# Optimization experiments

Hardware: AMD Instinct MI355X
Metric: run time of the kernel (lower is better)

Reference implementation:

```python
import jax, jax.numpy as jnp
import numpy as np

KS = 7
ITERS = 6
B, C, H, W = 2, 64, 256, 1216

_WM7 = [1,1,1,1,1,1,1,1,0,0,0,0,0,1,1,0,0,0,0,0,1,1,0,0,0,0,0,1,1,0,0,0,0,0,1,1,0,0,0,0,0,1,1,1,1,1,1,1,1]
_WM5 = [0,0,0,0,0,0,0,0,1,1,1,1,1,0,0,1,0,0,0,1,0,0,1,0,0,0,1,0,0,1,0,0,0,1,0,0,1,1,1,1,1,0,0,0,0,0,0,0,0]
_WM3 = [0,0,0,0,0,0,0,0,0,0,0,0,0,0,0,0,1,1,1,0,0,0,0,1,0,1,0,0,0,0,1,1,1,0,0,0,0,0,0,0,0,0,0,0,0,0,0,0,0]

# per 7x7 position t: which guide tensor (ring) and which channel within it
_SRC = []
_i7 = _i5 = _i3 = 0
for _t in range(KS * KS):
    if _WM7[_t]:
        _SRC.append(("7", _i7)); _i7 += 1
    elif _WM5[_t]:
        _SRC.append(("5", _i5)); _i5 += 1
    elif _WM3[_t]:
        _SRC.append(("3", _i3)); _i3 += 1
    else:
        _SRC.append(("1", 0))


def _convbn(x, w, s, b):
    # Conv2d(bias=False) + BatchNorm2d (inference) folded to per-channel scale/bias.
    y = jax.lax.conv_general_dilated(x, w, window_strides=(1, 1),
                                     padding=((1, 1), (1, 1)),
                                     dimension_numbers=("NCHW", "OIHW", "NCHW"))
    return y * s[None, :, None, None] + b[None, :, None, None]


def setup_inputs() -> dict:
    key = jax.random.key(0)
    ks = iter(jax.random.split(key, 64))
    def nrm(shape, scale=1.0):
        return jax.random.normal(next(ks), shape, jnp.float32) * scale
    def uni(shape):
        return jax.random.uniform(next(ks), shape, dtype=jnp.float32)
    inp = {
        "feature": nrm((B, C, H, W)),
        "d0": uni((B, 1, H, W)),
        "d00": nrm((B, 1, H, W)),  # ~half positive -> mixed valid_mask
    }
    layers = [("aff7", 24), ("aff5", 16), ("aff3", 8),
              ("att7", 6), ("att5", 6), ("att3", 6), ("att1", 6), ("mask", 6)]
    fan = 1.0 / np.sqrt(C * 9)
    for name, out in layers:
        inp["w_" + name] = nrm((out, C, 3, 3), fan)
        inp["s_" + name] = uni((out,))
        inp["b_" + name] = nrm((out,), 0.1)
    return inp


def reference(feature, d0, d00,
              w_aff7, s_aff7, b_aff7, w_aff5, s_aff5, b_aff5, w_aff3, s_aff3, b_aff3,
              w_att7, s_att7, b_att7, w_att5, s_att5, b_att5, w_att3, s_att3, b_att3,
              w_att1, s_att1, b_att1, w_mask, s_mask, b_mask):
    valid = (d00 > 0).astype(d00.dtype)
    mask_all = jax.nn.sigmoid(_convbn(feature, w_mask, s_mask, b_mask)) * valid
    aff7 = _convbn(feature, w_aff7, s_aff7, b_aff7)  # [B,24,H,W]
    aff5 = _convbn(feature, w_aff5, s_aff5, b_aff5)  # [B,16,H,W]
    aff3 = _convbn(feature, w_aff3, s_aff3, b_aff3)  # [B, 8,H,W]
    att7 = jax.nn.sigmoid(_convbn(feature, w_att7, s_att7, b_att7))
    att5 = jax.nn.sigmoid(_convbn(feature, w_att5, s_att5, b_att5))
    att3 = jax.nn.sigmoid(_convbn(feature, w_att3, s_att3, b_att3))
    att1 = jax.nn.sigmoid(_convbn(feature, w_att1, s_att1, b_att1))

    dt = d0
    for it in range(ITERS):
        mask = mask_all[:, it:it + 1]
        g7 = att7[:, it:it + 1] * aff7
        g5 = att5[:, it:it + 1] * aff5
        g3 = att3[:, it:it + 1] * aff3
        g1 = att1[:, it:it + 1]
        denom = (jnp.sum(jnp.abs(g7), 1, keepdims=True)
                 + jnp.sum(jnp.abs(g5), 1, keepdims=True)
                 + jnp.sum(jnp.abs(g3), 1, keepdims=True)
                 + jnp.abs(g1))
        g7, g5, g3, g1 = g7 / denom, g5 / denom, g3 / denom, g1 / denom
        g0 = 1.0 - (jnp.sum(g7, 1, keepdims=True) + jnp.sum(g5, 1, keepdims=True)
                    + jnp.sum(g3, 1, keepdims=True) + g1)
        guides = {"7": g7, "5": g5, "3": g3, "1": g1}
        # scatter ring guides into full 49-channel 7x7 layout
        G = jnp.concatenate([guides[k][:, i:i + 1] for k, i in _SRC], axis=1)  # [B,49,H,W]
        # weighted neighbor gather: out(p) = sum_t G_t(p+off_t) * dt(p+off_t)
        P = G * dt  # [B,49,H,W]
        Pp = jnp.pad(P, ((0, 0), (0, 0), (3, 3), (3, 3)))
        acc = jnp.zeros_like(dt)
        for t in range(KS * KS):
            i, j = t // KS, t % KS
            acc = acc + Pp[:, t:t + 1, 6 - i:6 - i + H, 6 - j:6 - j + W]
        dt = acc + g0 * d0
        dt = mask * d00 + (1.0 - mask) * dt
    return dt
```

## Files before the change

kernel.cpp:

```cpp
#include <hip/hip_runtime.h>
#include <hip/hip_fp16.h>
#include <stdint.h>

#define HH 256
#define WW 1216
#define BB 2
#define CC 64
#define IPIX (HH*WW)
#define NPIX (BB*IPIX)

typedef __attribute__((ext_vector_type(8))) __bf16 bf16x8;
typedef __attribute__((ext_vector_type(4))) __bf16 bf16x4;
typedef __attribute__((ext_vector_type(4))) float floatx4;
typedef __attribute__((ext_vector_type(4))) _Float16 half4;
typedef __attribute__((ext_vector_type(4))) uint32_t uint32x4;

__device__ __forceinline__ float sigm(float x) { return 1.f / (1.f + __expf(-x)); }

constexpr int LSTART_H[9] = {0,24,40,48,54,60,66,72,78};

constexpr int PLANE[49] = {
  0, 1, 2, 3, 4, 5, 6,
  7,24,25,26,27,28, 8,
  9,29,40,41,42,30,10,
 11,31,43,-1,44,32,12,
 13,33,45,46,47,34,14,
 15,35,36,37,38,39,16,
 17,18,19,20,21,22,23};
constexpr int KCLS[49] = {
 0,0,0,0,0,0,0,
 0,1,1,1,1,1,0,
 0,1,2,2,2,1,0,
 0,1,2,3,2,1,0,
 0,1,2,2,2,1,0,
 0,1,1,1,1,1,0,
 0,0,0,0,0,0,0};
constexpr int TAPNC[48] = {
  0,1,2,3,4,5,6,7,8,9,10,11,12,13,14,15,16,17,18,19,20,21,22,23,
  25,26,27,28,29,30,31,32,33,34,35,36,37,38,39,40,41,42,43,44,45,46,47,48};

struct WPtrs {
    const float* w[8];
    const float* s[8];
    const float* b[8];
};

__global__ void k_pack(WPtrs wp, __bf16* __restrict__ wpk,
                       float* __restrict__ s_all, float* __restrict__ b_all) {
    int idx = blockIdx.x * blockDim.x + threadIdx.x;
    if (idx < 18 * 5 * 64) {
        int kk = idx / (5 * 64);
        int r = idx - kk * 5 * 64;
        int t = r >> 6, lane = r & 63;
        int m = t * 16 + (lane & 15);
        int L = 0, o = 0;
        bool valid_m = (m < 78);
        if (valid_m) {
            for (int i = 0; i < 8; i++) if (m >= LSTART_H[i]) { L = i; o = m - LSTART_H[i]; }
        }
        __bf16 vals[8];
        for (int j = 0; j < 8; j++) {
            int k = kk * 32 + ((lane >> 4) * 8) + j;
            int tap = k >> 6, c = k & 63;
            float w = valid_m ? wp.w[L][(o * 64 + c) * 9 + tap] : 0.f;
            vals[j] = (__bf16)w;
        }
        for (int j = 0; j < 8; j++) wpk[(size_t)idx * 8 + j] = vals[j];
    }
    if (idx < 80) {
        int m = idx;
        float sv = 0.f, bv = 0.f;
        if (m < 78) {
            int L = 0, o = 0;
            for (int i = 0; i < 8; i++) if (m >= LSTART_H[i]) { L = i; o = m - LSTART_H[i]; }
            sv = wp.s[L][o]; bv = wp.b[L][o];
        }
        s_all[m] = sv; b_all[m] = bv;
    }
}

__global__ __launch_bounds__(256) void k_cvt(const float* __restrict__ feat,
                                             __bf16* __restrict__ fpk) {
    const int x = blockIdx.x * 64 + (threadIdx.x & 63);
    const int half = threadIdx.x >> 6;
    const int y = blockIdx.y, b = blockIdx.z;
    const float* fb = feat + (size_t)b * CC * IPIX + (size_t)y * WW + x;
    __bf16* op = fpk + ((size_t)(b * IPIX + y * WW + x) << 6);
#pragma unroll
    for (int h = 0; h < 2; h++) {
        const int cg = half + h * 4;
        bf16x8 pk;
#pragma unroll
        for (int j = 0; j < 8; j++) pk[j] = (__bf16)fb[(size_t)(cg * 8 + j) * IPIX];
        *(bf16x8*)(op + cg * 8) = pk;
    }
}

__global__ __launch_bounds__(256, 4) void k_conv(const __bf16* __restrict__ fpk,
        const float* __restrict__ d00, const __bf16* __restrict__ wpk,
        const float* __restrict__ s_all, const float* __restrict__ b_all,
        __bf16* __restrict__ afx, __bf16* __restrict__ attp, __bf16* __restrict__ maskp,
        float* __restrict__ stp) {
    __shared__ __bf16 sh[6 * 34 * 72];
    __shared__ __bf16 wlds[2 * 2560];
    const int tid = threadIdx.x;
    int flat = blockIdx.x + 38 * (blockIdx.y + 64 * blockIdx.z);
    int nf = (flat & 7) * 608 + (flat >> 3);
    int bx = nf % 38; int r2 = nf / 38;
    const int x0 = bx * 32, y0 = (r2 & 63) * 4, b = r2 >> 6;

    {
        bf16x8 w0 = *(const bf16x8*)(wpk + (size_t)tid * 8);
        *(bf16x8*)(wlds + tid * 8) = w0;
        if (tid < 64) {
            bf16x8 w1 = *(const bf16x8*)(wpk + 2048 + (size_t)tid * 8);
            *(bf16x8*)(wlds + 2048 + tid * 8) = w1;
        }
    }
    for (int idx = tid; idx < 204 * 8; idx += 256) {
        int cg = idx & 7, pos = idx >> 3;
        int row = pos / 34, x = pos - row * 34;
        int gy = y0 + row - 1, gx = x0 + x - 1;
        bf16x8 pk;
#pragma unroll
        for (int j = 0; j < 8; j++) pk[j] = (__bf16)0.f;
        if (gy >= 0 && gy < HH && gx >= 0 && gx < WW)
            pk = *(const bf16x8*)(fpk + ((size_t)(b * IPIX + gy * WW + gx) << 6) + cg * 8);
        *(bf16x8*)(sh + pos * 72 + cg * 8) = pk;
    }
    __syncthreads();

    const int wave = tid >> 6, lane = tid & 63;
    const int n = lane & 15, g = lane >> 4;

    floatx4 acc[5][2];
#pragma unroll
    for (int t = 0; t < 5; t++)
#pragma unroll
        for (int q = 0; q < 2; q++) acc[t][q] = (floatx4)(0.f);

#pragma unroll
    for (int kk = 0; kk < 18; kk++) {
        bf16x8 wt0, wt1;
        if (kk < 17) {
            wt0 = *(const bf16x8*)(wpk + (size_t)(kk + 1) * 2560 + tid * 8);
            if (tid < 64) wt1 = *(const bf16x8*)(wpk + (size_t)(kk + 1) * 2560 + 2048 + tid * 8);
        }
        const int tap = kk >> 1;
        const int dy = tap / 3 - 1, dx = tap % 3 - 1;
        const int c0 = (kk & 1) * 32 + g * 8;
        bf16x8 bfr[2];
        const int rowb = wave + 1 + dy;
        const int colb = 1 + dx + n;
#pragma unroll
        for (int q = 0; q < 2; q++)
            bfr[q] = *(const bf16x8*)(sh + ((rowb * 34) + colb + q * 16) * 72 + c0);
        bf16x8 afr[5];
        const __bf16* wb = wlds + (kk & 1) * 2560 + lane * 8;
#pragma unroll
        for (int t = 0; t < 5; t++) afr[t] = *(const bf16x8*)(wb + t * 512);
#pragma unroll
        for (int t = 0; t < 5; t++)
#pragma unroll
            for (int q = 0; q < 2; q++)
                acc[t][q] = __builtin_amdgcn_mfma_f32_16x16x32_bf16(afr[t], bfr[q], acc[t][q], 0, 0, 0);
        if (kk < 17) {
            *(bf16x8*)(wlds + ((kk + 1) & 1) * 2560 + tid * 8) = wt0;
            if (tid < 64) *(bf16x8*)(wlds + ((kk + 1) & 1) * 2560 + 2048 + tid * 8) = wt1;
        }
        __syncthreads();
    }

    const int pix_base = b * IPIX + (y0 + wave) * WW + x0 + n;
    float p7[2] = {0,0}, t7[2] = {0,0};
    float p5[2] = {0,0}, t5[2] = {0,0};
    float p3[2] = {0,0}, t3[2] = {0,0};

#pragma unroll
    for (int t = 0; t < 5; t++) {
        const floatx4 sv = *(const floatx4*)(s_all + t * 16 + 4 * g);
        const floatx4 bv = *(const floatx4*)(b_all + t * 16 + 4 * g);
#pragma unroll
        for (int q = 0; q < 2; q++) {
#pragma unroll
            for (int reg = 0; reg < 4; reg++) {
                const int m = t * 16 + 4 * g + reg;
                const float v = fmaf(acc[t][q][reg], sv[reg], bv[reg]);
                if (m < 24)                { p7[q] += fabsf(v); t7[q] += v; }
                else if (m < 40)           { p5[q] += fabsf(v); t5[q] += v; }
                else if (m < 48)           { p3[q] += fabsf(v); t3[q] += v; }
                const float outv = (m < 48) ? v : sigm(v);
                sh[m * 132 + wave * 32 + n + q * 16] = (__bf16)outv;
            }
        }
    }
#pragma unroll
    for (int q = 0; q < 2; q++) {
        p7[q] += __shfl_xor(p7[q], 16); p7[q] += __shfl_xor(p7[q], 32);
        t7[q] += __shfl_xor(t7[q], 16); t7[q] += __shfl_xor(t7[q], 32);
        p5[q] += __shfl_xor(p5[q], 16); p5[q] += __shfl_xor(p5[q], 32);
        t5[q] += __shfl_xor(t5[q], 16); t5[q] += __shfl_xor(t5[q], 32);
        p3[q] += __shfl_xor(p3[q], 16); p3[q] += __shfl_xor(p3[q], 32);
        t3[q] += __shfl_xor(t3[q], 16); t3[q] += __shfl_xor(t3[q], 32);
    }
    if (g == 0) {
#pragma unroll
        for (int q = 0; q < 2; q++) {
            const int pixq = pix_base + q * 16;
            floatx4 s0 = {p7[q], p5[q], p3[q], t7[q]};
            floatx4 s1 = {t5[q], t3[q], 0.f, 0.f};
            *(floatx4*)(stp + (size_t)pixq * 8)     = s0;
            *(floatx4*)(stp + (size_t)pixq * 8 + 4) = s1;
        }
    }
    __syncthreads();

    {
        const int pxi = tid >> 1;
        const int hf = tid & 1;
        const int prow2 = pxi >> 5, pcol2 = pxi & 31;
        const int pix2 = b * IPIX + (y0 + prow2) * WW + x0 + pcol2;
#pragma unroll
        for (int k = 0; k < 3; k++) {
            bf16x8 v;
#pragma unroll
            for (int e = 0; e < 8; e++) {
                const int jj = hf * 24 + k * 8 + e;
                v[e] = sh[PLANE[TAPNC[jj]] * 132 + pxi];
            }
            *(bf16x8*)(afx + (size_t)pix2 * 48 + hf * 24 + k * 8) = v;
        }
    }

    const int px = tid & 127;
    const int grp = tid >> 7;
    const int prow = px >> 5, pcol = px & 31;
    const int pix = b * IPIX + (y0 + prow) * WW + x0 + pcol;
    const float d00v = d00[pix];
    const float valid = (d00v > 0.f) ? 1.f : 0.f;
#pragma unroll
    for (int j = 0; j < 6; j += 2) {
        const int it = j + grp;
        bf16x4 av = { sh[(48 + it) * 132 + px], sh[(54 + it) * 132 + px],
                      sh[(60 + it) * 132 + px], sh[(66 + it) * 132 + px] };
        *(bf16x4*)(attp + ((size_t)it * NPIX + pix) * 4) = av;
        maskp[(size_t)it * NPIX + pix] = (__bf16)((float)sh[(72 + it) * 132 + px] * valid);
    }
}

__global__ __launch_bounds__(256) void k_rg(const __bf16* __restrict__ attp,
        const float* __restrict__ stp, const float* __restrict__ d0,
        _Float16* __restrict__ rp, float* __restrict__ gd) {
    int g = blockIdx.x * blockDim.x + threadIdx.x;
    if (g >= NPIX) return;
    const floatx4 s0 = *(const floatx4*)(stp + (size_t)g * 8);
    const floatx4 s1 = *(const floatx4*)(stp + (size_t)g * 8 + 4);
    const float S7 = s0[0], S5 = s0[1], S3 = s0[2], T7 = s0[3], T5 = s1[0], T3 = s1[1];
    const float d0v = d0[g];
#pragma unroll
    for (int it = 0; it < 6; it++) {
        bf16x4 a = *(const bf16x4*)(attp + ((size_t)it * NPIX + g) * 4);
        float a7 = (float)a[0], a5 = (float)a[1], a3 = (float)a[2], a1 = (float)a[3];
        float denom = a7 * S7 + a5 * S5 + a3 * S3 + a1;
        float inv = 1.f / denom;
        float r7 = a7 * inv, r5 = a5 * inv, r3 = a3 * inv, r1 = a1 * inv;
        float g0 = 1.f - (r7 * T7 + r5 * T5 + r3 * T3 + r1);
        half4 rv = {(_Float16)r7, (_Float16)r5, (_Float16)r3, (_Float16)r1};
        *(half4*)(rp + ((size_t)it * NPIX + g) * 4) = rv;
        gd[(size_t)it * NPIX + g] = g0 * d0v;
    }
}

#define SPP 536
__global__ __launch_bounds__(256) void k_iter(const _Float16* __restrict__ rp,
        const float* __restrict__ gd, const float* __restrict__ dt,
        const __bf16* __restrict__ afx, const __bf16* __restrict__ maskp,
        const float* __restrict__ d00,
        float* __restrict__ dtn, int it) {
    __shared__ uint32_t sa32[532 * 25];
    __shared__ float sps[4 * SPP];
    const int tid = threadIdx.x;
    int flat = blockIdx.x + 38 * (blockIdx.y + 32 * blockIdx.z);
    int nf = (flat & 7) * 304 + (flat >> 3);
    int bx = nf % 38; int r2 = nf / 38;
    const int x0 = bx * 32, y0 = (r2 & 31) * 8, b = r2 >> 5;
    const int ib = b * IPIX;

    for (int idx = tid; idx < 532; idx += 256) {
        const int ly = idx / 38, lx = idx - ly * 38;
        const int gy = y0 + ly - 3, gx = x0 + lx - 3;
        uint32x4 A[6];
        float c0 = 0.f, c1 = 0.f, c2 = 0.f, c3 = 0.f;
        if (gy >= 0 && gy < HH && gx >= 0 && gx < WW) {
            const int q = ib + gy * WW + gx;
            const uint32_t* src = (const uint32_t*)(afx + (size_t)q * 48);
#pragma unroll
            for (int k = 0; k < 6; k++) A[k] = *(const uint32x4*)(src + k * 4);
            const half4 rv = *(const half4*)(rp + ((size_t)it * NPIX + q) * 4);
            const float dtv = dt[q];
            const float gdv = gd[(size_t)it * NPIX + q];
            c0 = (float)rv[0] * dtv; c1 = (float)rv[1] * dtv;
            c2 = (float)rv[2] * dtv; c3 = (float)rv[3] * dtv + gdv;
        } else {
#pragma unroll
            for (int k = 0; k < 6; k++) A[k] = (uint32x4)(0u);
        }
        uint32_t* d = sa32 + idx * 25;
#pragma unroll
        for (int k = 0; k < 6; k++) {
            d[k * 4 + 0] = A[k][0]; d[k * 4 + 1] = A[k][1];
            d[k * 4 + 2] = A[k][2]; d[k * 4 + 3] = A[k][3];
        }
        sps[idx] = c0; sps[SPP + idx] = c1; sps[2 * SPP + idx] = c2; sps[3 * SPP + idx] = c3;
    }
    __syncthreads();

    const int ox = tid & 31, oy = tid >> 5;
    const int pbase = oy * 38 + ox;
    const __bf16* sab = (const __bf16*)sa32;
    float acc0 = sps[3 * SPP + pbase + 3 * 38 + 3];
    float acc1 = 0.f;
#pragma unroll
    for (int jj = 0; jj < 48; jj++) {
        const int t = TAPNC[jj];
        const int i = t / 7, j = t % 7;
        const int off = (6 - i) * 38 + (6 - j);
        const float av = (float)sab[(pbase + off) * 50 + jj];
        const float pv = sps[KCLS[t] * SPP + pbase + off];
        if (jj & 1) acc1 = fmaf(av, pv, acc1);
        else        acc0 = fmaf(av, pv, acc0);
    }
    const float acc = acc0 + acc1;

    const int pix = ib + (y0 + oy) * WW + (x0 + ox);
    const float m = (float)maskp[(size_t)it * NPIX + pix];
    dtn[pix] = m * d00[pix] + (1.f - m) * acc;
}

extern "C" void kernel_launch(void* const* d_in, const int* in_sizes, int n_in,
                              void* d_out, int out_size, void* d_ws, size_t ws_size,
                              hipStream_t stream) {
    const float* feat = (const float*)d_in[0];
    const float* d0   = (const float*)d_in[1];
    const float* d00  = (const float*)d_in[2];
    WPtrs wp;
    for (int l = 0; l < 8; l++) {
        wp.w[l] = (const float*)d_in[3 + 3 * l];
        wp.s[l] = (const float*)d_in[4 + 3 * l];
        wp.b[l] = (const float*)d_in[5 + 3 * l];
    }
    __bf16*   wsb   = (__bf16*)d_ws;
    __bf16*   afx   = wsb;
    __bf16*   attp  = afx + (size_t)48 * NPIX;
    __bf16*   msk_b = attp + (size_t)24 * NPIX;
    float*    stp   = (float*)(msk_b + (size_t)6 * NPIX);
    float*    dtA   = stp + (size_t)8 * NPIX;
    __bf16*   wpk   = (__bf16*)(dtA + (size_t)NPIX);
    float*    s_all = (float*)(wpk + 18 * 5 * 64 * 8);
    float*    b_all = s_all + 80;
    char*     X     = (char*)(b_all + 80);
    __bf16*   fpk   = (__bf16*)X;
    _Float16* rp    = (_Float16*)X;
    float*    gd    = (float*)(X + (size_t)24 * NPIX * 2);
    float*    dtB   = (float*)d_out;

    hipLaunchKernelGGL(k_pack, dim3(23), dim3(256), 0, stream, wp, wpk, s_all, b_all);
    hipLaunchKernelGGL(k_cvt, dim3(WW / 64, HH, BB), dim3(256), 0, stream, feat, fpk);
    hipLaunchKernelGGL(k_conv, dim3(38, 64, 2), dim3(256), 0, stream,
                       fpk, d00, wpk, s_all, b_all, afx, attp, msk_b, stp);
    hipLaunchKernelGGL(k_rg, dim3(NPIX / 256), dim3(256), 0, stream,
                       attp, stp, d0, rp, gd);
    const float* cur = d0;
    for (int it = 0; it < 6; ++it) {
        float* nxt = (it & 1) ? dtB : dtA;
        if (it == 5) nxt = dtB;
        hipLaunchKernelGGL(k_iter, dim3(38, 32, 2), dim3(256), 0, stream,
                           rp, gd, cur, afx, msk_b, d00, nxt, it);
        cur = nxt;
    }
}
```

Measured before the change: 559.0 us.

## Scatter affinities into destination-pixel layout so iterations read them directly

The conv kernel now writes each affinity tap to the output pixel that will consume it (the shifted neighbour position) instead of to the source pixel. Each propagation iteration can then load its 48 affinities as six contiguous vectors from global memory into registers, which removes the 532-entry LDS staging of the affinity halo and its large shared-memory footprint. A new kernel zeros the border records that no conv tap writes, and the iteration loop gains four accumulators. The cost is scattered 2-byte global stores in the conv kernel, traded for cheaper, higher-occupancy iteration kernels that run six times.

```diff
diff --git a/kernel.cpp b/kernel.cpp
--- a/kernel.cpp
+++ b/kernel.cpp
@@ -79,6 +79,29 @@
     }
 }
 
+__global__ __launch_bounds__(256) void k_zero_afy(__bf16* __restrict__ afy) {
+    const int idx = blockIdx.x * blockDim.x + threadIdx.x;
+    const int total = 2 * 8796 * 6;
+    if (idx >= total) return;
+    const int part = idx % 6;
+    const int rec = idx / 6;
+    const int r = rec % 8796;
+    const int b = rec / 8796;
+    int y, x;
+    if (r < 7296) {
+        const int yy = r / 1216;
+        y = (yy < 3) ? yy : (250 + yy);
+        x = r - yy * 1216;
+    } else {
+        const int r2 = r - 7296;
+        y = 3 + r2 / 6;
+        const int c = r2 % 6;
+        x = (c < 3) ? c : (1210 + c);
+    }
+    uint32x4 z = (uint32x4)(0u);
+    *(uint32x4*)((uint32_t*)(afy + ((size_t)(b * IPIX + y * WW + x)) * 48) + part * 4) = z;
+}
+
 __global__ __launch_bounds__(256) void k_cvt(const float* __restrict__ feat,
                                              __bf16* __restrict__ fpk) {
     const int x = blockIdx.x * 64 + (threadIdx.x & 63);
@@ -99,7 +122,7 @@
 __global__ __launch_bounds__(256, 4) void k_conv(const __bf16* __restrict__ fpk,
         const float* __restrict__ d00, const __bf16* __restrict__ wpk,
         const float* __restrict__ s_all, const float* __restrict__ b_all,
-        __bf16* __restrict__ afx, __bf16* __restrict__ attp, __bf16* __restrict__ maskp,
+        __bf16* __restrict__ afy, __bf16* __restrict__ attp, __bf16* __restrict__ maskp,
         float* __restrict__ stp) {
     __shared__ __bf16 sh[6 * 34 * 72];
     __shared__ __bf16 wlds[2 * 2560];
@@ -219,16 +242,16 @@
         const int pxi = tid >> 1;
         const int hf = tid & 1;
         const int prow2 = pxi >> 5, pcol2 = pxi & 31;
-        const int pix2 = b * IPIX + (y0 + prow2) * WW + x0 + pcol2;
-#pragma unroll
-        for (int k = 0; k < 3; k++) {
-            bf16x8 v;
-#pragma unroll
-            for (int e = 0; e < 8; e++) {
-                const int jj = hf * 24 + k * 8 + e;
-                v[e] = sh[PLANE[TAPNC[jj]] * 132 + pxi];
-            }
-            *(bf16x8*)(afx + (size_t)pix2 * 48 + hf * 24 + k * 8) = v;
+        const int gy = y0 + prow2, gx = x0 + pcol2;
+#pragma unroll
+        for (int k = 0; k < 24; k++) {
+            const int jj = hf * 24 + k;
+            const int t = TAPNC[jj];
+            const int i = t / 7, j = t % 7;
+            const int oy = gy + i - 3, ox = gx + j - 3;
+            const __bf16 v = sh[PLANE[t] * 132 + pxi];
+            if (oy >= 0 && oy < HH && ox >= 0 && ox < WW)
+                afy[((size_t)(b * IPIX + oy * WW + ox)) * 48 + jj] = v;
         }
     }
 
@@ -274,10 +297,9 @@
 #define SPP 536
 __global__ __launch_bounds__(256) void k_iter(const _Float16* __restrict__ rp,
         const float* __restrict__ gd, const float* __restrict__ dt,
-        const __bf16* __restrict__ afx, const __bf16* __restrict__ maskp,
+        const __bf16* __restrict__ afy, const __bf16* __restrict__ maskp,
         const float* __restrict__ d00,
         float* __restrict__ dtn, int it) {
-    __shared__ uint32_t sa32[532 * 25];
     __shared__ float sps[4 * SPP];
     const int tid = threadIdx.x;
     int flat = blockIdx.x + 38 * (blockIdx.y + 32 * blockIdx.z);
@@ -289,50 +311,46 @@
     for (int idx = tid; idx < 532; idx += 256) {
         const int ly = idx / 38, lx = idx - ly * 38;
         const int gy = y0 + ly - 3, gx = x0 + lx - 3;
-        uint32x4 A[6];
         float c0 = 0.f, c1 = 0.f, c2 = 0.f, c3 = 0.f;
         if (gy >= 0 && gy < HH && gx >= 0 && gx < WW) {
             const int q = ib + gy * WW + gx;
-            const uint32_t* src = (const uint32_t*)(afx + (size_t)q * 48);
-#pragma unroll
-            for (int k = 0; k < 6; k++) A[k] = *(const uint32x4*)(src + k * 4);
             const half4 rv = *(const half4*)(rp + ((size_t)it * NPIX + q) * 4);
             const float dtv = dt[q];
             const float gdv = gd[(size_t)it * NPIX + q];
             c0 = (float)rv[0] * dtv; c1 = (float)rv[1] * dtv;
             c2 = (float)rv[2] * dtv; c3 = (float)rv[3] * dtv + gdv;
-        } else {
-#pragma unroll
-            for (int k = 0; k < 6; k++) A[k] = (uint32x4)(0u);
-        }
-        uint32_t* d = sa32 + idx * 25;
-#pragma unroll
-        for (int k = 0; k < 6; k++) {
-            d[k * 4 + 0] = A[k][0]; d[k * 4 + 1] = A[k][1];
-            d[k * 4 + 2] = A[k][2]; d[k * 4 + 3] = A[k][3];
         }
         sps[idx] = c0; sps[SPP + idx] = c1; sps[2 * SPP + idx] = c2; sps[3 * SPP + idx] = c3;
     }
+
+    const int ox = tid & 31, oy = tid >> 5;
+    const int pix = ib + (y0 + oy) * WW + (x0 + ox);
+    bf16x8 A[6];
+    const __bf16* ar = afy + (size_t)pix * 48;
+#pragma unroll
+    for (int k = 0; k < 6; k++) A[k] = *(const bf16x8*)(ar + k * 8);
+
     __syncthreads();
 
-    const int ox = tid & 31, oy = tid >> 5;
     const int pbase = oy * 38 + ox;
-    const __bf16* sab = (const __bf16*)sa32;
     float acc0 = sps[3 * SPP + pbase + 3 * 38 + 3];
-    float acc1 = 0.f;
+    float acc1 = 0.f, acc2 = 0.f, acc3 = 0.f;
 #pragma unroll
     for (int jj = 0; jj < 48; jj++) {
         const int t = TAPNC[jj];
         const int i = t / 7, j = t % 7;
         const int off = (6 - i) * 38 + (6 - j);
-        const float av = (float)sab[(pbase + off) * 50 + jj];
+        const float av = (float)A[jj >> 3][jj & 7];
         const float pv = sps[KCLS[t] * SPP + pbase + off];
-        if (jj & 1) acc1 = fmaf(av, pv, acc1);
-        else        acc0 = fmaf(av, pv, acc0);
-    }
-    const float acc = acc0 + acc1;
-
-    const int pix = ib + (y0 + oy) * WW + (x0 + ox);
+        switch (jj & 3) {
+            case 0: acc0 = fmaf(av, pv, acc0); break;
+            case 1: acc1 = fmaf(av, pv, acc1); break;
+            case 2: acc2 = fmaf(av, pv, acc2); break;
+            default: acc3 = fmaf(av, pv, acc3); break;
+        }
+    }
+    const float acc = (acc0 + acc1) + (acc2 + acc3);
+
     const float m = (float)maskp[(size_t)it * NPIX + pix];
     dtn[pix] = m * d00[pix] + (1.f - m) * acc;
 }
@@ -350,8 +368,8 @@
         wp.b[l] = (const float*)d_in[5 + 3 * l];
     }
     __bf16*   wsb   = (__bf16*)d_ws;
-    __bf16*   afx   = wsb;
-    __bf16*   attp  = afx + (size_t)48 * NPIX;
+    __bf16*   afy   = wsb;
+    __bf16*   attp  = afy + (size_t)48 * NPIX;
     __bf16*   msk_b = attp + (size_t)24 * NPIX;
     float*    stp   = (float*)(msk_b + (size_t)6 * NPIX);
     float*    dtA   = stp + (size_t)8 * NPIX;
@@ -365,9 +383,10 @@
     float*    dtB   = (float*)d_out;
 
     hipLaunchKernelGGL(k_pack, dim3(23), dim3(256), 0, stream, wp, wpk, s_all, b_all);
+    hipLaunchKernelGGL(k_zero_afy, dim3((2 * 8796 * 6 + 255) / 256), dim3(256), 0, stream, afy);
     hipLaunchKernelGGL(k_cvt, dim3(WW / 64, HH, BB), dim3(256), 0, stream, feat, fpk);
     hipLaunchKernelGGL(k_conv, dim3(38, 64, 2), dim3(256), 0, stream,
-                       fpk, d00, wpk, s_all, b_all, afx, attp, msk_b, stp);
+                       fpk, d00, wpk, s_all, b_all, afy, attp, msk_b, stp);
     hipLaunchKernelGGL(k_rg, dim3(NPIX / 256), dim3(256), 0, stream,
                        attp, stp, d0, rp, gd);
     const float* cur = d0;
@@ -375,7 +394,7 @@
         float* nxt = (it & 1) ? dtB : dtA;
         if (it == 5) nxt = dtB;
         hipLaunchKernelGGL(k_iter, dim3(38, 32, 2), dim3(256), 0, stream,
-                           rp, gd, cur, afx, msk_b, d00, nxt, it);
+                           rp, gd, cur, afy, msk_b, d00, nxt, it);
         cur = nxt;
     }
 }
```

Result: slower. 606.6 us (+8.5%).
